# Performance work log

Hardware: AMD Instinct MI355X
Metric: run time of the kernel (lower is better)

Reference implementation:

```python
import jax, jax.numpy as jnp
import numpy as np

N_IN = 2_000_000
N_OUT = 250_000
K = 8          # 2x2x2 octree kernel, stride 2
C_IN = 32
C_OUT = 64
BN_EPS = 1e-5


def setup_inputs() -> dict:
    key = jax.random.key(0)
    k1, k2, k3, k4, k5 = jax.random.split(key, 5)
    data = jax.random.normal(k1, (N_IN, C_IN), dtype=jnp.float32)
    # Octree neighbor table: index of each of the 8 children of every output
    # octant; -1 marks an empty child (nempty=True).
    neigh = jax.random.randint(k2, (N_OUT, K), 0, N_IN, dtype=jnp.int32)
    empty = jax.random.uniform(k3, (N_OUT, K)) < 0.2
    neigh = jnp.where(empty, -1, neigh)
    # Conv weight [K*C_IN, C_OUT] + bias, BatchNorm affine params.
    scale = 1.0 / np.sqrt(K * C_IN)
    weight = jax.random.normal(k4, (K * C_IN, C_OUT), dtype=jnp.float32) * scale
    bias = jnp.zeros((C_OUT,), dtype=jnp.float32)
    gamma = jnp.ones((C_OUT,), dtype=jnp.float32)
    beta = jnp.zeros((C_OUT,), dtype=jnp.float32)
    return {"data": data, "weight": weight, "bias": bias,
            "gamma": gamma, "beta": beta, "neigh": neigh}


def reference(data, weight, bias, gamma, beta, neigh):
    # --- OctreeConv stride-2, kernel 2x2x2, nempty=True ---
    valid = (neigh >= 0)                               # [N_OUT, K]
    idx = jnp.where(valid, neigh, 0)
    gathered = data[idx] * valid[..., None].astype(data.dtype)  # [N_OUT, K, C_IN]
    out = gathered.reshape(gathered.shape[0], -1) @ weight + bias  # [N_OUT, C_OUT]
    # --- BatchNorm1d (training: batch stats, biased variance) ---
    mean = jnp.mean(out, axis=0)
    var = jnp.var(out, axis=0)
    out = (out - mean) * jax.lax.rsqrt(var + BN_EPS) * gamma + beta
    return out
```

## Files before the change

kernel.cpp:

```cpp
#include <hip/hip_runtime.h>
#include <hip/hip_bf16.h>

#define C_INC   32
#define C_OUTC  64
#define KNBR    8
#define BN_EPS  1e-5f

#define BT_STRIDE 264
#define NB_PAD 1024

typedef __bf16 bf16x8 __attribute__((ext_vector_type(8)));
typedef float  floatx4 __attribute__((ext_vector_type(4)));

__device__ inline unsigned short f2bf_bits(float f) {
    unsigned int u = __builtin_bit_cast(unsigned int, f);
    unsigned int r = (u + 0x7FFFu + ((u >> 16) & 1u)) >> 16;
    return (unsigned short)r;
}
__device__ inline __bf16 f2bf(float f) {
    return __builtin_bit_cast(__bf16, f2bf_bits(f));
}

__global__ __launch_bounds__(256) void conv_kernel(
    const float* __restrict__ data,
    const float* __restrict__ weight,
    const float* __restrict__ bias,
    const int*   __restrict__ neigh,
    float*       __restrict__ out,
    float*       __restrict__ partialsT,
    int n_out)
{
    __shared__ unsigned short Bt[C_OUTC * BT_STRIDE];
    __shared__ float red[2 * C_OUTC];

    const int t    = threadIdx.x;
    const int lane = t & 63;
    const int wave = t >> 6;
    const int m16  = lane & 15;
    const int q    = lane >> 4;

    if (t < 2 * C_OUTC) red[t] = 0.0f;

    {
        const int n = t & 63;
        const int g = t >> 6;
        #pragma unroll 8
        for (int kk = 0; kk < 64; ++kk) {
            int k = kk * 4 + g;
            Bt[n * BT_STRIDE + k] = f2bf_bits(weight[k * C_OUTC + n]);
        }
    }
    __syncthreads();

    float biasv[4];
    #pragma unroll
    for (int nt = 0; nt < 4; ++nt) biasv[nt] = bias[nt * 16 + m16];

    float s1[4] = {0.f, 0.f, 0.f, 0.f};
    float s2[4] = {0.f, 0.f, 0.f, 0.f};

    const int rowBase = blockIdx.x * 256;
    const int4* __restrict__ neigh4 = reinterpret_cast<const int4*>(neigh);

    for (int pass = 0; pass < 4; ++pass) {
        const int tile0 = rowBase + pass * 64 + wave * 16;
        if (tile0 >= n_out) continue;

        floatx4 acc[4];
        #pragma unroll
        for (int nt = 0; nt < 4; ++nt) acc[nt] = (floatx4){0.f, 0.f, 0.f, 0.f};

        const int arow = tile0 + m16;

        const int4 nA = neigh4[(size_t)arow * 2 + 0];
        const int4 nB = neigh4[(size_t)arow * 2 + 1];
        int nidxs[KNBR] = {nA.x, nA.y, nA.z, nA.w, nB.x, nB.y, nB.z, nB.w};

        float4 g0[KNBR], g1[KNBR];
        #pragma unroll
        for (int ks = 0; ks < KNBR; ++ks) {
            g0[ks] = (float4){0.f, 0.f, 0.f, 0.f};
            g1[ks] = (float4){0.f, 0.f, 0.f, 0.f};
            if (nidxs[ks] >= 0) {
                const float4* p = reinterpret_cast<const float4*>(
                    data + (size_t)nidxs[ks] * C_INC + q * 8);
                g0[ks] = p[0];
                g1[ks] = p[1];
            }
        }

        #pragma unroll
        for (int ks = 0; ks < KNBR; ++ks) {
            bf16x8 a;
            a[0] = f2bf(g0[ks].x); a[1] = f2bf(g0[ks].y);
            a[2] = f2bf(g0[ks].z); a[3] = f2bf(g0[ks].w);
            a[4] = f2bf(g1[ks].x); a[5] = f2bf(g1[ks].y);
            a[6] = f2bf(g1[ks].z); a[7] = f2bf(g1[ks].w);

            #pragma unroll
            for (int nt = 0; nt < 4; ++nt) {
                const bf16x8 b = *reinterpret_cast<const bf16x8*>(
                    &Bt[(nt * 16 + m16) * BT_STRIDE + ks * 32 + q * 8]);
                acc[nt] = __builtin_amdgcn_mfma_f32_16x16x32_bf16(a, b, acc[nt], 0, 0, 0);
            }
        }

        #pragma unroll
        for (int nt = 0; nt < 4; ++nt) {
            const int c = nt * 16 + m16;
            #pragma unroll
            for (int r = 0; r < 4; ++r) {
                const int drow = tile0 + q * 4 + r;
                const float v = acc[nt][r] + biasv[nt];
                out[(size_t)drow * C_OUTC + c] = v;
                s1[nt] += v;
                s2[nt] += v * v;
            }
        }
    }

    #pragma unroll
    for (int nt = 0; nt < 4; ++nt) {
        #pragma unroll
        for (int off = 16; off < 64; off <<= 1) {
            s1[nt] += __shfl_xor(s1[nt], off, 64);
            s2[nt] += __shfl_xor(s2[nt], off, 64);
        }
    }
    if (q == 0) {
        #pragma unroll
        for (int nt = 0; nt < 4; ++nt) {
            const int c = nt * 16 + m16;
            atomicAdd(&red[c], s1[nt]);
            atomicAdd(&red[C_OUTC + c], s2[nt]);
        }
    }
    __syncthreads();
    if (t < 2 * C_OUTC) {
        partialsT[(size_t)t * NB_PAD + blockIdx.x] = red[t];
    }
}

__global__ __launch_bounds__(256) void stats_kernel(
    const float* __restrict__ partialsT, int nb,
    const float* __restrict__ gamma, const float* __restrict__ beta,
    float* __restrict__ ab, int n_out)
{
    const int t    = threadIdx.x;
    const int lane = t & 63;
    const int wave = t >> 6;
    const int c    = blockIdx.x;

    float sA = 0.f, sB = 0.f;
    for (int b = t; b < nb; b += 256) {
        sA += partialsT[(size_t)c * NB_PAD + b];
        sB += partialsT[(size_t)(C_OUTC + c) * NB_PAD + b];
    }
    #pragma unroll
    for (int off = 1; off < 64; off <<= 1) {
        sA += __shfl_xor(sA, off, 64);
        sB += __shfl_xor(sB, off, 64);
    }
    __shared__ float red[8];
    if (lane == 0) { red[wave] = sA; red[4 + wave] = sB; }
    __syncthreads();
    if (t == 0) {
        const float S1 = (red[0] + red[1]) + (red[2] + red[3]);
        const float S2 = (red[4] + red[5]) + (red[6] + red[7]);
        const float invN = 1.0f / (float)n_out;
        const float mean = S1 * invN;
        const float var  = S2 * invN - mean * mean;
        const float rstd = rsqrtf(var + BN_EPS);
        const float a    = gamma[c] * rstd;
        ab[c]          = a;
        ab[C_OUTC + c] = beta[c] - mean * a;
    }
}

__global__ __launch_bounds__(256) void bn_kernel(
    float* __restrict__ out, const float* __restrict__ ab, long n4)
{
    const long i = (long)blockIdx.x * blockDim.x + threadIdx.x;
    if (i >= n4) return;
    const int c4 = (int)(i & 15);
    float4 v = reinterpret_cast<float4*>(out)[i];
    const float4 a  = reinterpret_cast<const float4*>(ab)[c4];
    const float4 bb = reinterpret_cast<const float4*>(ab + C_OUTC)[c4];
    v.x = v.x * a.x + bb.x;
    v.y = v.y * a.y + bb.y;
    v.z = v.z * a.z + bb.z;
    v.w = v.w * a.w + bb.w;
    reinterpret_cast<float4*>(out)[i] = v;
}

extern "C" void kernel_launch(void* const* d_in, const int* in_sizes, int n_in,
                              void* d_out, int out_size, void* d_ws, size_t ws_size,
                              hipStream_t stream) {
    const float* data   = (const float*)d_in[0];
    const float* weight = (const float*)d_in[1];
    const float* bias   = (const float*)d_in[2];
    const float* gamma  = (const float*)d_in[3];
    const float* beta   = (const float*)d_in[4];
    const int*   neigh  = (const int*)d_in[5];

    const int n_out = in_sizes[5] / KNBR;
    float* out = (float*)d_out;

    const int nb = (n_out + 255) / 256;

    float* partialsT = (float*)d_ws;
    float* ab = partialsT + (size_t)128 * NB_PAD;

    hipLaunchKernelGGL(conv_kernel, dim3(nb), dim3(256), 0, stream,
                       data, weight, bias, neigh, out, partialsT, n_out);
    hipLaunchKernelGGL(stats_kernel, dim3(C_OUTC), dim3(256), 0, stream,
                       partialsT, nb, gamma, beta, ab, n_out);
    const long n4 = (long)n_out * C_OUTC / 4;
    hipLaunchKernelGGL(bn_kernel, dim3((unsigned)((n4 + 255) / 256)), dim3(256), 0, stream,
                       out, ab, n4);
}
```

Before: 381.5 us.

## Double rows per block, prefetch neighbor indices, drop bias, use native bf16 cast

Each block now covers 512 rows in 8 passes instead of 256, which halves the number of blocks and amortizes the per-block weight staging into LDS. The neighbor indices for the next pass are prefetched while the current pass runs, and the first load is issued before the weight staging. The bias add is removed, since batch-norm mean subtraction cancels a per-channel bias exactly. The manual rounding helper is replaced with the compiler's native bf16 conversion. Halving the block count (about 489 blocks) may reduce occupancy and latency hiding for the gather.

```diff
diff --git a/kernel.cpp b/kernel.cpp
--- a/kernel.cpp
+++ b/kernel.cpp
@@ -8,6 +8,8 @@
 
 #define BT_STRIDE 264
 #define NB_PAD 1024
+#define ROWS_PER_BLOCK 512
+#define NPASS 8
 
 typedef __bf16 bf16x8 __attribute__((ext_vector_type(8)));
 typedef float  floatx4 __attribute__((ext_vector_type(4)));
@@ -18,13 +20,12 @@
     return (unsigned short)r;
 }
 __device__ inline __bf16 f2bf(float f) {
-    return __builtin_bit_cast(__bf16, f2bf_bits(f));
+    return (__bf16)f;
 }
 
 __global__ __launch_bounds__(256) void conv_kernel(
     const float* __restrict__ data,
     const float* __restrict__ weight,
-    const float* __restrict__ bias,
     const int*   __restrict__ neigh,
     float*       __restrict__ out,
     float*       __restrict__ partialsT,
@@ -41,6 +42,17 @@
 
     if (t < 2 * C_OUTC) red[t] = 0.0f;
 
+    const int rowBase = blockIdx.x * ROWS_PER_BLOCK;
+    const int4* __restrict__ neigh4 = reinterpret_cast<const int4*>(neigh);
+
+    int4 nA, nB;
+    {
+        const int arow = rowBase + wave * 16 + m16;
+        const int ar = arow < n_out ? arow : 0;
+        nA = neigh4[(size_t)ar * 2 + 0];
+        nB = neigh4[(size_t)ar * 2 + 1];
+    }
+
     {
         const int n = t & 63;
         const int g = t >> 6;
@@ -52,29 +64,27 @@
     }
     __syncthreads();
 
-    float biasv[4];
-    #pragma unroll
-    for (int nt = 0; nt < 4; ++nt) biasv[nt] = bias[nt * 16 + m16];
-
     float s1[4] = {0.f, 0.f, 0.f, 0.f};
     float s2[4] = {0.f, 0.f, 0.f, 0.f};
 
-    const int rowBase = blockIdx.x * 256;
-    const int4* __restrict__ neigh4 = reinterpret_cast<const int4*>(neigh);
-
-    for (int pass = 0; pass < 4; ++pass) {
+    for (int pass = 0; pass < NPASS; ++pass) {
         const int tile0 = rowBase + pass * 64 + wave * 16;
+
+        const int4 cA = nA, cB = nB;
+        if (pass < NPASS - 1) {
+            const int arow = rowBase + (pass + 1) * 64 + wave * 16 + m16;
+            const int ar = arow < n_out ? arow : 0;
+            nA = neigh4[(size_t)ar * 2 + 0];
+            nB = neigh4[(size_t)ar * 2 + 1];
+        }
+
         if (tile0 >= n_out) continue;
 
         floatx4 acc[4];
         #pragma unroll
         for (int nt = 0; nt < 4; ++nt) acc[nt] = (floatx4){0.f, 0.f, 0.f, 0.f};
 
-        const int arow = tile0 + m16;
-
-        const int4 nA = neigh4[(size_t)arow * 2 + 0];
-        const int4 nB = neigh4[(size_t)arow * 2 + 1];
-        int nidxs[KNBR] = {nA.x, nA.y, nA.z, nA.w, nB.x, nB.y, nB.z, nB.w};
+        int nidxs[KNBR] = {cA.x, cA.y, cA.z, cA.w, cB.x, cB.y, cB.z, cB.w};
 
         float4 g0[KNBR], g1[KNBR];
         #pragma unroll
@@ -111,7 +121,7 @@
             #pragma unroll
             for (int r = 0; r < 4; ++r) {
                 const int drow = tile0 + q * 4 + r;
-                const float v = acc[nt][r] + biasv[nt];
+                const float v = acc[nt][r];
                 out[(size_t)drow * C_OUTC + c] = v;
                 s1[nt] += v;
                 s2[nt] += v * v;
@@ -198,7 +208,6 @@
                               hipStream_t stream) {
     const float* data   = (const float*)d_in[0];
     const float* weight = (const float*)d_in[1];
-    const float* bias   = (const float*)d_in[2];
     const float* gamma  = (const float*)d_in[3];
     const float* beta   = (const float*)d_in[4];
     const int*   neigh  = (const int*)d_in[5];
@@ -206,13 +215,13 @@
     const int n_out = in_sizes[5] / KNBR;
     float* out = (float*)d_out;
 
-    const int nb = (n_out + 255) / 256;
+    const int nb = (n_out + ROWS_PER_BLOCK - 1) / ROWS_PER_BLOCK;
 
     float* partialsT = (float*)d_ws;
     float* ab = partialsT + (size_t)128 * NB_PAD;
 
     hipLaunchKernelGGL(conv_kernel, dim3(nb), dim3(256), 0, stream,
-                       data, weight, bias, neigh, out, partialsT, n_out);
+                       data, weight, neigh, out, partialsT, n_out);
     hipLaunchKernelGGL(stats_kernel, dim3(C_OUTC), dim3(256), 0, stream,
                        partialsT, nb, gamma, beta, ab, n_out);
     const long n4 = (long)n_out * C_OUTC / 4;
```

Result: no change. 386.9 us (+1.4%).
